# Optimization experiments

Hardware: AMD Instinct MI355X
Metric: run time of the kernel (lower is better)

The kernel has to match this reference:

```python
import jax, jax.numpy as jnp
import numpy as np

N = 1_000_000
D = 128

def setup_inputs() -> dict:
    key = jax.random.key(0)
    ks = jax.random.split(key, 20)
    inp = {}
    inp['atom_idx'] = jax.random.randint(ks[0], (N,), 0, 46)
    inp['degree_idx'] = jax.random.randint(ks[1], (N,), 0, 6)
    inp['charge_idx'] = jax.random.randint(ks[2], (N,), 0, 11)
    inp['hybrid_idx'] = jax.random.randint(ks[3], (N,), 0, 3)
    inp['numh_idx'] = jax.random.randint(ks[4], (N,), 0, 5)
    inp['chiral_idx'] = jax.random.randint(ks[5], (N,), 0, 4)
    inp['bond_counts'] = jax.random.randint(ks[6], (N, 4), 0, 5)  # counts in [0,4]
    inp['scalar3'] = jax.random.uniform(ks[7], (N, 3), dtype=jnp.float32)  # aromatic, in_ring, mass/100
    inp['E_atom'] = jax.random.normal(ks[8], (46, D), dtype=jnp.float32)
    inp['E_deg'] = jax.random.normal(ks[9], (6, D), dtype=jnp.float32)
    inp['E_chg'] = jax.random.normal(ks[10], (11, D), dtype=jnp.float32)
    inp['E_hyb'] = jax.random.normal(ks[11], (3, D), dtype=jnp.float32)
    inp['E_h'] = jax.random.normal(ks[12], (5, D), dtype=jnp.float32)
    inp['E_chi'] = jax.random.normal(ks[13], (4, D), dtype=jnp.float32)
    inp['E_bond'] = jax.random.normal(ks[14], (5, D), dtype=jnp.float32)
    inp['W'] = jax.random.normal(ks[15], (7, D), dtype=jnp.float32) * 0.1
    inp['b'] = jax.random.normal(ks[16], (D,), dtype=jnp.float32) * 0.1
    return inp


def reference(atom_idx, degree_idx, charge_idx, hybrid_idx, numh_idx, chiral_idx,
              bond_counts, scalar3, E_atom, E_deg, E_chg, E_hyb, E_h, E_chi,
              E_bond, W, b):
    # Sum of the six categorical embedding lookups -> [N, D]
    emb = (E_atom[atom_idx] + E_deg[degree_idx] + E_chg[charge_idx]
           + E_hyb[hybrid_idx] + E_h[numh_idx] + E_chi[chiral_idx])
    # Bond-context: for each of the 4 bond types, if count>0 add E_bond[count]
    bc = E_bond[bond_counts]                      # [N, 4, D]
    mask = (bond_counts > 0)[..., None]           # [N, 4, 1]
    emb = emb + jnp.where(mask, bc, 0.0).sum(axis=1)
    # Scalar features: [aromatic, in_ring, mass] ++ bond_counts/4 -> [N, 7]
    scal = jnp.concatenate([scalar3, bond_counts.astype(jnp.float32) / 4.0], axis=-1)
    emb = emb + scal @ W + b
    return emb
```

## Files before the change

### kernel.cpp

```cpp
#include <hip/hip_runtime.h>

typedef float f4 __attribute__((ext_vector_type(4)));
typedef int   i4 __attribute__((ext_vector_type(4)));

static constexpr int D = 128;
static constexpr int NR_ATOM = 46, NR_DEG = 6, NR_CHG = 11, NR_HYB = 3,
                     NR_H = 5, NR_CHI = 4, NR_BOND = 5;

static constexpr int OFF_ATOM = 0;
static constexpr int OFF_DEG  = OFF_ATOM + NR_ATOM * D;
static constexpr int OFF_CHG  = OFF_DEG  + NR_DEG  * D;
static constexpr int OFF_HYB  = OFF_CHG  + NR_CHG  * D;
static constexpr int OFF_H    = OFF_HYB  + NR_HYB  * D;
static constexpr int OFF_CHI  = OFF_H    + NR_H    * D;
static constexpr int OFF_BOND = OFF_CHI  + NR_CHI  * D;
static constexpr int OFF_W    = OFF_BOND + NR_BOND * D;
static constexpr int OFF_B    = OFF_W    + 7 * D;
static constexpr int LDS_FLOATS = OFF_B + D;

__global__ __launch_bounds__(512, 6)
void atom_featurizer_kernel(const int*   __restrict__ atom_idx,
                            const int*   __restrict__ degree_idx,
                            const int*   __restrict__ charge_idx,
                            const int*   __restrict__ hybrid_idx,
                            const int*   __restrict__ numh_idx,
                            const int*   __restrict__ chiral_idx,
                            const int*   __restrict__ bond_counts,
                            const float* __restrict__ scalar3,
                            const float* __restrict__ E_atom,
                            const float* __restrict__ E_deg,
                            const float* __restrict__ E_chg,
                            const float* __restrict__ E_hyb,
                            const float* __restrict__ E_h,
                            const float* __restrict__ E_chi,
                            const float* __restrict__ E_bond,
                            const float* __restrict__ W,
                            const float* __restrict__ b,
                            float*       __restrict__ out,
                            int N)
{
    __shared__ float lds[LDS_FLOATS];
    const int tid = threadIdx.x;

    {
        const float* srcs[9] = {E_atom, E_deg, E_chg, E_hyb, E_h, E_chi, E_bond, W, b};
        const int    offs[9] = {OFF_ATOM, OFF_DEG, OFF_CHG, OFF_HYB, OFF_H, OFF_CHI,
                                OFF_BOND, OFF_W, OFF_B};
        const int    cnts[9] = {NR_ATOM*D, NR_DEG*D, NR_CHG*D, NR_HYB*D, NR_H*D,
                                NR_CHI*D, NR_BOND*D, 7*D, D};
        for (int t = 0; t < 9; ++t) {
            const f4* s = (const f4*)srcs[t];
            f4* d = (f4*)(lds + offs[t]);
            const int n4 = cnts[t] >> 2;
            for (int i = tid; i < n4; i += 512) d[i] = s[i];
        }
    }
    __syncthreads();

    const int lane = tid & 31;
    const int grp  = tid >> 5;
    const int d0   = lane << 2;
    const int groupsPerBlock = 512 >> 5;
    const int totalGroups = (int)gridDim.x * groupsPerBlock;

    auto ld = [&](int off) -> f4 { return *(const f4*)(lds + off + d0); };

    f4 w0 = ld(OFF_W + 0*D), w1 = ld(OFF_W + 1*D), w2 = ld(OFF_W + 2*D),
       w3 = ld(OFF_W + 3*D), w4 = ld(OFF_W + 4*D), w5 = ld(OFF_W + 5*D),
       w6 = ld(OFF_W + 6*D);
    f4 bias = ld(OFF_B);

    for (int n = (int)blockIdx.x * groupsPerBlock + grp; n < N; n += totalGroups) {
        const int ia  = atom_idx[n];
        const int ide = degree_idx[n];
        const int ic  = charge_idx[n];
        const int ih  = hybrid_idx[n];
        const int inh = numh_idx[n];
        const int ix  = chiral_idx[n];
        const i4  bc  = *(const i4*)(bond_counts + 4 * (size_t)n);
        const float s0 = scalar3[3 * (size_t)n + 0];
        const float s1 = scalar3[3 * (size_t)n + 1];
        const float s2 = scalar3[3 * (size_t)n + 2];

        f4 acc = ld(OFF_ATOM + ia * D);
        acc += ld(OFF_DEG + ide * D);
        acc += ld(OFF_CHG + ic  * D);
        acc += ld(OFF_HYB + ih  * D);
        acc += ld(OFF_H   + inh * D);
        acc += ld(OFF_CHI + ix  * D);

        const float m0 = bc.x > 0 ? 1.0f : 0.0f;
        const float m1 = bc.y > 0 ? 1.0f : 0.0f;
        const float m2 = bc.z > 0 ? 1.0f : 0.0f;
        const float m3 = bc.w > 0 ? 1.0f : 0.0f;
        acc += m0 * ld(OFF_BOND + bc.x * D);
        acc += m1 * ld(OFF_BOND + bc.y * D);
        acc += m2 * ld(OFF_BOND + bc.z * D);
        acc += m3 * ld(OFF_BOND + bc.w * D);

        acc += s0 * w0;
        acc += s1 * w1;
        acc += s2 * w2;
        acc += ((float)bc.x * 0.25f) * w3;
        acc += ((float)bc.y * 0.25f) * w4;
        acc += ((float)bc.z * 0.25f) * w5;
        acc += ((float)bc.w * 0.25f) * w6;
        acc += bias;

        __builtin_nontemporal_store(acc, (f4*)(out + (size_t)n * D + d0));
    }
}

extern "C" void kernel_launch(void* const* d_in, const int* in_sizes, int n_in,
                              void* d_out, int out_size, void* d_ws, size_t ws_size,
                              hipStream_t stream) {
    const int*   atom_idx    = (const int*)d_in[0];
    const int*   degree_idx  = (const int*)d_in[1];
    const int*   charge_idx  = (const int*)d_in[2];
    const int*   hybrid_idx  = (const int*)d_in[3];
    const int*   numh_idx    = (const int*)d_in[4];
    const int*   chiral_idx  = (const int*)d_in[5];
    const int*   bond_counts = (const int*)d_in[6];
    const float* scalar3     = (const float*)d_in[7];
    const float* E_atom      = (const float*)d_in[8];
    const float* E_deg       = (const float*)d_in[9];
    const float* E_chg       = (const float*)d_in[10];
    const float* E_hyb       = (const float*)d_in[11];
    const float* E_h         = (const float*)d_in[12];
    const float* E_chi       = (const float*)d_in[13];
    const float* E_bond      = (const float*)d_in[14];
    const float* W           = (const float*)d_in[15];
    const float* b           = (const float*)d_in[16];
    float*       out         = (float*)d_out;
    const int N = in_sizes[0];

    atom_featurizer_kernel<<<768, 512, 0, stream>>>(
        atom_idx, degree_idx, charge_idx, hybrid_idx, numh_idx, chiral_idx,
        bond_counts, scalar3, E_atom, E_deg, E_chg, E_hyb, E_h, E_chi, E_bond,
        W, b, out, N);
}
```

Measured before the change: 621.0 us.

## Prefetch next row indices, keep small tables in registers, count bond types

Each loop iteration now loads the index and scalar data for the next row while it computes the current one, so global load latency overlaps with the LDS gathers and the store. E_hyb, E_bond, W and b move out of LDS into per-thread registers, with the hybrid row picked by select and the bond terms computed as per-type counts times a register vector. Two accumulators split the dependency chain, and the grid drops to 512 blocks with launch bounds lowered to 4 blocks per CU. The cost is higher register pressure and possibly lower occupancy for a kernel that is mostly bound by output bandwidth.

```diff
diff --git a/kernel.cpp b/kernel.cpp
--- a/kernel.cpp
+++ b/kernel.cpp
@@ -4,21 +4,44 @@
 typedef int   i4 __attribute__((ext_vector_type(4)));
 
 static constexpr int D = 128;
-static constexpr int NR_ATOM = 46, NR_DEG = 6, NR_CHG = 11, NR_HYB = 3,
-                     NR_H = 5, NR_CHI = 4, NR_BOND = 5;
-
+static constexpr int NR_ATOM = 46, NR_DEG = 6, NR_CHG = 11, NR_H = 5, NR_CHI = 4;
 static constexpr int OFF_ATOM = 0;
 static constexpr int OFF_DEG  = OFF_ATOM + NR_ATOM * D;
 static constexpr int OFF_CHG  = OFF_DEG  + NR_DEG  * D;
-static constexpr int OFF_HYB  = OFF_CHG  + NR_CHG  * D;
-static constexpr int OFF_H    = OFF_HYB  + NR_HYB  * D;
+static constexpr int OFF_H    = OFF_CHG  + NR_CHG  * D;
 static constexpr int OFF_CHI  = OFF_H    + NR_H    * D;
-static constexpr int OFF_BOND = OFF_CHI  + NR_CHI  * D;
-static constexpr int OFF_W    = OFF_BOND + NR_BOND * D;
-static constexpr int OFF_B    = OFF_W    + 7 * D;
-static constexpr int LDS_FLOATS = OFF_B + D;
+static constexpr int LDS_FLOATS = OFF_CHI + NR_CHI * D;
 
-__global__ __launch_bounds__(512, 6)
+struct Idx {
+    int ia, ide, ic, ih, inh, ix;
+    i4 bc;
+    float s0, s1, s2;
+};
+
+__device__ __forceinline__ Idx load_idx(const int* __restrict__ atom_idx,
+                                        const int* __restrict__ degree_idx,
+                                        const int* __restrict__ charge_idx,
+                                        const int* __restrict__ hybrid_idx,
+                                        const int* __restrict__ numh_idx,
+                                        const int* __restrict__ chiral_idx,
+                                        const int* __restrict__ bond_counts,
+                                        const float* __restrict__ scalar3,
+                                        int n) {
+    Idx r;
+    r.ia  = atom_idx[n];
+    r.ide = degree_idx[n];
+    r.ic  = charge_idx[n];
+    r.ih  = hybrid_idx[n];
+    r.inh = numh_idx[n];
+    r.ix  = chiral_idx[n];
+    r.bc  = *(const i4*)(bond_counts + 4 * (size_t)n);
+    r.s0  = scalar3[3 * (size_t)n + 0];
+    r.s1  = scalar3[3 * (size_t)n + 1];
+    r.s2  = scalar3[3 * (size_t)n + 2];
+    return r;
+}
+
+__global__ __launch_bounds__(512, 4)
 void atom_featurizer_kernel(const int*   __restrict__ atom_idx,
                             const int*   __restrict__ degree_idx,
                             const int*   __restrict__ charge_idx,
@@ -43,71 +66,87 @@
     const int tid = threadIdx.x;
 
     {
-        const float* srcs[9] = {E_atom, E_deg, E_chg, E_hyb, E_h, E_chi, E_bond, W, b};
-        const int    offs[9] = {OFF_ATOM, OFF_DEG, OFF_CHG, OFF_HYB, OFF_H, OFF_CHI,
-                                OFF_BOND, OFF_W, OFF_B};
-        const int    cnts[9] = {NR_ATOM*D, NR_DEG*D, NR_CHG*D, NR_HYB*D, NR_H*D,
-                                NR_CHI*D, NR_BOND*D, 7*D, D};
-        for (int t = 0; t < 9; ++t) {
+        const float* srcs[5] = {E_atom, E_deg, E_chg, E_h, E_chi};
+        const int    offs[5] = {OFF_ATOM, OFF_DEG, OFF_CHG, OFF_H, OFF_CHI};
+        const int    cnts[5] = {NR_ATOM*D, NR_DEG*D, NR_CHG*D, NR_H*D, NR_CHI*D};
+        for (int t = 0; t < 5; ++t) {
             const f4* s = (const f4*)srcs[t];
             f4* d = (f4*)(lds + offs[t]);
             const int n4 = cnts[t] >> 2;
             for (int i = tid; i < n4; i += 512) d[i] = s[i];
         }
     }
-    __syncthreads();
 
     const int lane = tid & 31;
     const int grp  = tid >> 5;
     const int d0   = lane << 2;
-    const int groupsPerBlock = 512 >> 5;
-    const int totalGroups = (int)gridDim.x * groupsPerBlock;
+    const int stride = (int)gridDim.x * 16;
 
-    auto ld = [&](int off) -> f4 { return *(const f4*)(lds + off + d0); };
+    auto ldg = [&](const float* p, int row) -> f4 {
+        return *(const f4*)(p + row * D + d0);
+    };
+    const f4 w0 = ldg(W,0), w1 = ldg(W,1), w2 = ldg(W,2), w3 = ldg(W,3),
+             w4 = ldg(W,4), w5 = ldg(W,5), w6 = ldg(W,6);
+    const f4 bias = *(const f4*)(b + d0);
+    const f4 eb1 = ldg(E_bond,1), eb2 = ldg(E_bond,2),
+             eb3 = ldg(E_bond,3), eb4 = ldg(E_bond,4);
+    const f4 hy0 = ldg(E_hyb,0), hy1 = ldg(E_hyb,1), hy2 = ldg(E_hyb,2);
 
-    f4 w0 = ld(OFF_W + 0*D), w1 = ld(OFF_W + 1*D), w2 = ld(OFF_W + 2*D),
-       w3 = ld(OFF_W + 3*D), w4 = ld(OFF_W + 4*D), w5 = ld(OFF_W + 5*D),
-       w6 = ld(OFF_W + 6*D);
-    f4 bias = ld(OFF_B);
+    __syncthreads();
 
-    for (int n = (int)blockIdx.x * groupsPerBlock + grp; n < N; n += totalGroups) {
-        const int ia  = atom_idx[n];
-        const int ide = degree_idx[n];
-        const int ic  = charge_idx[n];
-        const int ih  = hybrid_idx[n];
-        const int inh = numh_idx[n];
-        const int ix  = chiral_idx[n];
-        const i4  bc  = *(const i4*)(bond_counts + 4 * (size_t)n);
-        const float s0 = scalar3[3 * (size_t)n + 0];
-        const float s1 = scalar3[3 * (size_t)n + 1];
-        const float s2 = scalar3[3 * (size_t)n + 2];
+    auto ldl = [&](int off) -> f4 { return *(const f4*)(lds + off + d0); };
 
-        f4 acc = ld(OFF_ATOM + ia * D);
-        acc += ld(OFF_DEG + ide * D);
-        acc += ld(OFF_CHG + ic  * D);
-        acc += ld(OFF_HYB + ih  * D);
-        acc += ld(OFF_H   + inh * D);
-        acc += ld(OFF_CHI + ix  * D);
+    int n = (int)blockIdx.x * 16 + grp;
+    if (n >= N) return;
 
-        const float m0 = bc.x > 0 ? 1.0f : 0.0f;
-        const float m1 = bc.y > 0 ? 1.0f : 0.0f;
-        const float m2 = bc.z > 0 ? 1.0f : 0.0f;
-        const float m3 = bc.w > 0 ? 1.0f : 0.0f;
-        acc += m0 * ld(OFF_BOND + bc.x * D);
-        acc += m1 * ld(OFF_BOND + bc.y * D);
-        acc += m2 * ld(OFF_BOND + bc.z * D);
-        acc += m3 * ld(OFF_BOND + bc.w * D);
+    Idx cur = load_idx(atom_idx, degree_idx, charge_idx, hybrid_idx, numh_idx,
+                       chiral_idx, bond_counts, scalar3, n);
 
-        acc += s0 * w0;
-        acc += s1 * w1;
-        acc += s2 * w2;
-        acc += ((float)bc.x * 0.25f) * w3;
-        acc += ((float)bc.y * 0.25f) * w4;
-        acc += ((float)bc.z * 0.25f) * w5;
-        acc += ((float)bc.w * 0.25f) * w6;
-        acc += bias;
+    while (true) {
+        const int nn = n + stride;
+        const bool more = nn < N;
+        Idx nxt = load_idx(atom_idx, degree_idx, charge_idx, hybrid_idx,
+                           numh_idx, chiral_idx, bond_counts, scalar3,
+                           more ? nn : n);
 
-        __builtin_nontemporal_store(acc, (f4*)(out + (size_t)n * D + d0));
+        const i4 bc = cur.bc;
+
+        f4 a0 = ldl(OFF_ATOM + cur.ia  * D);
+        f4 a1 = ldl(OFF_DEG  + cur.ide * D);
+        a0 += ldl(OFF_CHG + cur.ic  * D);
+        a1 += ldl(OFF_H   + cur.inh * D);
+        a0 += ldl(OFF_CHI + cur.ix  * D);
+
+        a1 += (cur.ih == 0) ? hy0 : ((cur.ih == 1) ? hy1 : hy2);
+
+        const int c1 = (bc.x==1)+(bc.y==1)+(bc.z==1)+(bc.w==1);
+        const int c2 = (bc.x==2)+(bc.y==2)+(bc.z==2)+(bc.w==2);
+        const int c3 = (bc.x==3)+(bc.y==3)+(bc.z==3)+(bc.w==3);
+        const int c4 = (bc.x==4)+(bc.y==4)+(bc.z==4)+(bc.w==4);
+        a0 += (float)c1 * eb1;
+        a1 += (float)c2 * eb2;
+        a0 += (float)c3 * eb3;
+        a1 += (float)c4 * eb4;
+
+        a0 += cur.s0 * w0;
+        a1 += cur.s1 * w1;
+        a0 += cur.s2 * w2;
+        const float t0 = (float)bc.x * 0.25f;
+        const float t1 = (float)bc.y * 0.25f;
+        const float t2 = (float)bc.z * 0.25f;
+        const float t3 = (float)bc.w * 0.25f;
+        a0 += t0 * w3;
+        a1 += t1 * w4;
+        a0 += t2 * w5;
+        a1 += t3 * w6;
+        a0 += bias;
+
+        const f4 r = a0 + a1;
+        __builtin_nontemporal_store(r, (f4*)(out + (size_t)n * D + d0));
+
+        if (!more) break;
+        cur = nxt;
+        n = nn;
     }
 }
 
@@ -134,7 +173,7 @@
     float*       out         = (float*)d_out;
     const int N = in_sizes[0];
 
-    atom_featurizer_kernel<<<768, 512, 0, stream>>>(
+    atom_featurizer_kernel<<<512, 512, 0, stream>>>(
         atom_idx, degree_idx, charge_idx, hybrid_idx, numh_idx, chiral_idx,
         bond_counts, scalar3, E_atom, E_deg, E_chg, E_hyb, E_h, E_chi, E_bond,
         W, b, out, N);
```

After: 650.3 us. +4.7%, slower.
